# Optimization experiments

Hardware: AMD Instinct MI355X
Metric: run time of the kernel (lower is better)

Reference implementation:

```python
import jax, jax.numpy as jnp
import numpy as np

POOL = 7
SUB = 2
C = 256
NUM_CLASS = 81
N_ROIS = 1000
IMG = 1024


def _roi_align(feat, rois, img_size, pool=POOL, sub=SUB):
    # feat: (1, C, H, W); rois: (N, 4) as (y1, x1, y2, x2) in image coords
    H, W = feat.shape[2], feat.shape[3]
    fhw = jnp.array([H, W, H, W], jnp.float32) - 1.0
    im = jnp.concatenate([img_size, img_size]).astype(jnp.float32) - 1.0
    rif = rois * fhw / im  # rois mapped into feature-map coords
    S = pool * sub  # subsampled grid per axis (14)
    h_step = (rif[:, 2] - rif[:, 0]) / S  # (N,)
    w_step = (rif[:, 3] - rif[:, 1]) / S
    grid = jnp.arange(S, dtype=jnp.float32) + 0.5
    ys = grid[None, :] * h_step[:, None] + rif[:, 0:1]  # (N, S)
    xs = grid[None, :] * w_step[:, None] + rif[:, 1:2]  # (N, S)
    cy = ys[:, :, None]  # (N, S, 1) -> broadcast (N, S, S)
    cx = xs[:, None, :]  # (N, 1, S)
    iu = jnp.floor(cy)
    il = jnp.floor(cx)
    ly = cy - iu  # frac parts (bilinear weights)
    lx = cx - il
    iu = iu.astype(jnp.int32)
    il = il.astype(jnp.int32)
    idn = jnp.ceil(cy).astype(jnp.int32)
    ir = jnp.ceil(cx).astype(jnp.int32)
    iu = jnp.broadcast_to(iu, (rois.shape[0], S, S))
    idn = jnp.broadcast_to(idn, (rois.shape[0], S, S))
    il = jnp.broadcast_to(il, (rois.shape[0], S, S))
    ir = jnp.broadcast_to(ir, (rois.shape[0], S, S))
    f = feat[0]  # (C, H, W)
    # fancy-index gather of 4 corners: each (C, N, S, S)
    pre = (f[:, iu, il] * (1 - ly) * (1 - lx)
           + f[:, idn, il] * ly * (1 - lx)
           + f[:, iu, ir] * (1 - ly) * lx
           + f[:, idn, ir] * ly * lx)
    pre = pre.transpose(1, 0, 2, 3)  # (N, C, S, S)
    N = rois.shape[0]
    post = pre.reshape(N, f.shape[0], pool, sub, pool, sub).max(axis=(3, 5))
    return post  # (N, C, pool, pool)


def _pyramid_roi_pool(feats, rois, img_size):
    h = rois[:, 2] - rois[:, 0] + 1
    w = rois[:, 3] - rois[:, 1] + 1
    lvl = jnp.floor(jnp.log(jnp.sqrt(h * w) / 224.0) / 0.693147 + 4.0)
    lvl = jnp.clip(lvl, 2.0, 5.0)
    # compute ROIAlign against each level, select per-roi by mask
    out = jnp.zeros((rois.shape[0], C, POOL, POOL), jnp.float32)
    for i, l in enumerate(range(2, 6)):
        pooled = _roi_align(feats[i], rois, img_size)
        mask = (lvl == l)[:, None, None, None]
        out = jnp.where(mask, pooled, out)
    return out


def setup_inputs() -> dict:
    key = jax.random.key(0)
    ks = jax.random.split(key, 10)
    feat2 = jax.random.normal(ks[0], (1, C, 256, 256), jnp.float32)
    feat3 = jax.random.normal(ks[1], (1, C, 128, 128), jnp.float32)
    feat4 = jax.random.normal(ks[2], (1, C, 64, 64), jnp.float32)
    feat5 = jax.random.normal(ks[3], (1, C, 32, 32), jnp.float32)
    # valid boxes: log-uniform sizes in [32, 512] to cover levels 2..5
    u = jax.random.uniform(ks[4], (N_ROIS, 4))
    sh = jnp.exp(jnp.log(32.0) + u[:, 0] * (jnp.log(512.0) - jnp.log(32.0)))
    sw = jnp.exp(jnp.log(32.0) + u[:, 1] * (jnp.log(512.0) - jnp.log(32.0)))
    y1 = u[:, 2] * (IMG - 1 - sh)
    x1 = u[:, 3] * (IMG - 1 - sw)
    rois = jnp.stack([y1, x1, y1 + sh, x1 + sw], axis=1).astype(jnp.float32)
    img_size = jnp.array([IMG, IMG], jnp.int32)
    D = C * POOL * POOL  # 12544
    W1 = jax.random.normal(ks[5], (D, 1024), jnp.float32) * 0.01
    b1 = jnp.zeros((1024,), jnp.float32)
    W2 = jax.random.normal(ks[6], (1024, 1024), jnp.float32) * 0.01
    b2 = jnp.zeros((1024,), jnp.float32)
    Wloc = jax.random.normal(ks[7], (1024, NUM_CLASS * 4), jnp.float32) * 0.001
    bloc = jnp.zeros((NUM_CLASS * 4,), jnp.float32)
    Wsc = jax.random.normal(ks[8], (1024, NUM_CLASS), jnp.float32) * 0.01
    bsc = jnp.zeros((NUM_CLASS,), jnp.float32)
    return {"feat2": feat2, "feat3": feat3, "feat4": feat4, "feat5": feat5,
            "rois": rois, "img_size": img_size,
            "W1": W1, "b1": b1, "W2": W2, "b2": b2,
            "Wloc": Wloc, "bloc": bloc, "Wsc": Wsc, "bsc": bsc}


def reference(feat2, feat3, feat4, feat5, rois, img_size,
              W1, b1, W2, b2, Wloc, bloc, Wsc, bsc):
    pooled = _pyramid_roi_pool([feat2, feat3, feat4, feat5], rois, img_size)
    x = pooled.reshape(pooled.shape[0], -1)  # (N, 12544)
    fc = jax.nn.relu(x @ W1 + b1)
    fc = jax.nn.relu(fc @ W2 + b2)
    roi_cls_locs = fc @ Wloc + bloc
    roi_scores = fc @ Wsc + bsc
    return roi_cls_locs, roi_scores
```

## Files before the change

### kernel.cpp

```cpp
#include <hip/hip_runtime.h>
#include <hip/hip_bf16.h>
#include <cstdint>
#include <cstddef>

typedef __bf16 bf16x8 __attribute__((ext_vector_type(8)));
typedef float floatx4 __attribute__((ext_vector_type(4)));

#define NROIS 1000
#define PD    12544
#define K2_1  25088
#define FC_N  1024
#define K2_2  2048
#define NLOC  324
#define NSC   81
#define NH    405

#define OFF_FT   0u
#define OFF_W1T  0u
#define OFF_PART 12845056u
#define OFF_T2   0u
#define OFF_T3   16777216u
#define OFF_T4   20971520u
#define OFF_T5   22020096u
#define OFF_POOL 22282240u
#define OFF_W2T  35127296u
#define OFF_WHT  36175872u
#define OFF_FC1  36700160u
#define OFF_FC2  37748736u

__device__ __forceinline__ unsigned short f2bf(float x) {
    unsigned int u = __float_as_uint(x);
    u = u + 0x7fffu + ((u >> 16) & 1u);
    return (unsigned short)(u >> 16);
}
__device__ __forceinline__ float bf2f(unsigned short h) {
    return __uint_as_float(((unsigned int)h) << 16);
}
__device__ __forceinline__ ushort2 split_hl(float f) {
    const unsigned short hi = f2bf(f);
    const unsigned short lo = f2bf(f - bf2f(hi));
    return make_ushort2(hi, lo);
}

__global__ __launch_bounds__(256) void transpose_feat_kernel(
    const float* __restrict__ f2, const float* __restrict__ f3,
    const float* __restrict__ f4, const float* __restrict__ f5,
    float* __restrict__ fT)
{
    __shared__ float tile[64][65];
    int bx = blockIdx.x;
    const float* src; float* dst; int P;
    if (bx < 1024)      {            src = f2; dst = fT + OFF_T2; P = 65536; }
    else if (bx < 1280) { bx -= 1024; src = f3; dst = fT + OFF_T3; P = 16384; }
    else if (bx < 1344) { bx -= 1280; src = f4; dst = fT + OFF_T4; P = 4096; }
    else                { bx -= 1344; src = f5; dst = fT + OFF_T5; P = 1024; }

    const int p0  = bx * 64;
    const int c0  = blockIdx.y * 64;
    const int col = threadIdx.x & 63;
    const int r0  = threadIdx.x >> 6;
#pragma unroll
    for (int r = r0; r < 64; r += 4)
        tile[r][col] = src[(size_t)(c0 + r) * P + p0 + col];
    __syncthreads();
#pragma unroll
    for (int r = r0; r < 64; r += 4)
        dst[(size_t)(p0 + r) * 256 + c0 + col] = tile[col][r];
}

__global__ __launch_bounds__(256) void roi_pool_kernel(
    const float* __restrict__ fT, const float* __restrict__ rois,
    const int* __restrict__ img_size, ushort2* __restrict__ pooledHL)
{
    const int roi = blockIdx.x;
    const int ph  = blockIdx.y;
    const int c   = threadIdx.x;

    const float y1 = rois[roi * 4 + 0];
    const float x1 = rois[roi * 4 + 1];
    const float y2 = rois[roi * 4 + 2];
    const float x2 = rois[roi * 4 + 3];

    const float hh = y2 - y1 + 1.0f;
    const float ww = x2 - x1 + 1.0f;
    float lvlf = floorf(logf(sqrtf(hh * ww) / 224.0f) / 0.693147f + 4.0f);
    lvlf = fminf(fmaxf(lvlf, 2.0f), 5.0f);
    const int lvl = (int)lvlf;

    const float* f;
    int H;
    if (lvl == 2)      { f = fT + OFF_T2; H = 256; }
    else if (lvl == 3) { f = fT + OFF_T3; H = 128; }
    else if (lvl == 4) { f = fT + OFF_T4; H = 64;  }
    else               { f = fT + OFF_T5; H = 32;  }
    const int W = H;

    const float imh = (float)img_size[0] - 1.0f;
    const float imw = (float)img_size[1] - 1.0f;
    const float r0 = y1 * (float)(H - 1) / imh;
    const float r1 = x1 * (float)(W - 1) / imw;
    const float r2 = y2 * (float)(H - 1) / imh;
    const float r3 = x2 * (float)(W - 1) / imw;
    const float hs  = (r2 - r0) * (1.0f / 14.0f);
    const float wst = (r3 - r1) * (1.0f / 14.0f);

    float m[7];
#pragma unroll
    for (int i = 0; i < 7; ++i) m[i] = -INFINITY;

#pragma unroll
    for (int syy = 0; syy < 2; ++syy) {
        const float cy = ((float)(ph * 2 + syy) + 0.5f) * hs + r0;
        const float fy = floorf(cy);
        int   iu  = (int)fy;
        int   idn = (int)ceilf(cy);
        const float ly = cy - fy;
        iu  = min(max(iu, 0),  H - 1);
        idn = min(max(idn, 0), H - 1);
        const float wU = 1.0f - ly, wD = ly;
        const float* rowU = f + (size_t)(iu  * W) * 256;
        const float* rowD = f + (size_t)(idn * W) * 256;

#pragma unroll
        for (int sx = 0; sx < 14; ++sx) {
            const float cx = ((float)sx + 0.5f) * wst + r1;
            const float fx = floorf(cx);
            int   il = (int)fx;
            int   ir = (int)ceilf(cx);
            const float lx = cx - fx;
            il = min(max(il, 0), W - 1);
            ir = min(max(ir, 0), W - 1);

            const float v00 = rowU[il * 256 + c];
            const float v01 = rowU[ir * 256 + c];
            const float v10 = rowD[il * 256 + c];
            const float v11 = rowD[ir * 256 + c];
            const float v = (v00 * (1.0f - lx) + v01 * lx) * wU
                          + (v10 * (1.0f - lx) + v11 * lx) * wD;
            m[sx >> 1] = fmaxf(m[sx >> 1], v);
        }
    }

    ushort2* outRow = pooledHL + (size_t)roi * PD + c;
#pragma unroll
    for (int pw = 0; pw < 7; ++pw)
        outRow[(ph * 7 + pw) * 256] = split_hl(m[pw]);
}

__global__ __launch_bounds__(256) void convert_w1_kernel(
    const float* __restrict__ W1, ushort2* __restrict__ W1T)
{
    __shared__ float tile[64][65];
    const int p0  = blockIdx.x * 64;
    const int n0  = blockIdx.y * 64;
    const int col = threadIdx.x & 63;
    const int r0  = threadIdx.x >> 6;
#pragma unroll
    for (int r = r0; r < 64; r += 4) {
        const int pp   = p0 + r;
        const int ksrc = (pp & 255) * 49 + (pp >> 8);
        tile[r][col] = W1[(size_t)ksrc * 1024 + n0 + col];
    }
    __syncthreads();
#pragma unroll
    for (int nr = r0; nr < 64; nr += 4)
        W1T[(size_t)(n0 + nr) * PD + p0 + col] = split_hl(tile[col][nr]);
}

__global__ __launch_bounds__(256) void convert_w2h_kernel(
    const float* __restrict__ W2, const float* __restrict__ Wloc,
    const float* __restrict__ Wsc, ushort2* __restrict__ W2T,
    ushort2* __restrict__ WhT)
{
    __shared__ float tile[64][65];
    const int p0  = blockIdx.x * 64;
    const int col = threadIdx.x & 63;
    const int r0  = threadIdx.x >> 6;

    if (blockIdx.y < 16) {
        const int n0 = blockIdx.y * 64;
#pragma unroll
        for (int r = r0; r < 64; r += 4)
            tile[r][col] = W2[(size_t)(p0 + r) * 1024 + n0 + col];
        __syncthreads();
#pragma unroll
        for (int nr = r0; nr < 64; nr += 4)
            W2T[(size_t)(n0 + nr) * 1024 + p0 + col] = split_hl(tile[col][nr]);
    } else {
        const int n0 = (blockIdx.y - 16) * 64;
#pragma unroll
        for (int r = r0; r < 64; r += 4) {
            const int pp = p0 + r;
            const int n  = n0 + col;
            float v = 0.0f;
            if (n < NLOC)    v = Wloc[(size_t)pp * NLOC + n];
            else if (n < NH) v = Wsc[(size_t)pp * NSC + (n - NLOC)];
            tile[r][col] = v;
        }
        __syncthreads();
#pragma unroll
        for (int nr = r0; nr < 64; nr += 4)
            WhT[(size_t)(n0 + nr) * 1024 + p0 + col] = split_hl(tile[col][nr]);
    }
}

__global__ __launch_bounds__(256, 4) void gemm_bf16_kernel(
    const unsigned short* __restrict__ A,
    const unsigned short* __restrict__ B,
    float* __restrict__ partial,
    int K2, int N, int kLen)
{
    __shared__ __align__(16) unsigned short As[64 * 64];
    __shared__ __align__(16) unsigned short Bs[128 * 64];

    const int tid  = threadIdx.x;
    const int lane = tid & 63;
    const int wave = tid >> 6;
    const int kStart = blockIdx.x * kLen;
    const int n0 = blockIdx.y * 128;
    const int m0 = blockIdx.z * 64;

    const int rIn  = lane >> 3;
    const int cSrc = (lane & 7) ^ rIn;

    const int mrow = lane & 15, quad = lane >> 4;

    floatx4 acc[8];
#pragma unroll
    for (int j = 0; j < 8; ++j)
        acc[j] = (floatx4){0.f, 0.f, 0.f, 0.f};

    for (int k0 = kStart; k0 < kStart + kLen; k0 += 64) {
#pragma unroll
        for (int q = 0; q < 2; ++q) {
            const int rowBase = wave * 16 + q * 8;
            const unsigned short* ga =
                A + (size_t)(m0 + rowBase + rIn) * K2 + k0 + cSrc * 8;
            __builtin_amdgcn_global_load_lds(
                (const __attribute__((address_space(1))) void*)ga,
                (__attribute__((address_space(3))) void*)&As[rowBase * 64], 16, 0, 0);
        }
#pragma unroll
        for (int q = 0; q < 4; ++q) {
            const int rowBase = wave * 32 + q * 8;
            const unsigned short* gb =
                B + (size_t)(n0 + rowBase + rIn) * K2 + k0 + cSrc * 8;
            __builtin_amdgcn_global_load_lds(
                (const __attribute__((address_space(1))) void*)gb,
                (__attribute__((address_space(3))) void*)&Bs[rowBase * 64], 16, 0, 0);
        }
        __syncthreads();

#pragma unroll
        for (int ks = 0; ks < 2; ++ks) {
            const int ra = wave * 16 + mrow;
            const int ca = ((ks * 4 + quad) ^ (ra & 7)) * 8;
            const bf16x8 aF = *reinterpret_cast<const bf16x8*>(&As[ra * 64 + ca]);
#pragma unroll
            for (int j = 0; j < 8; ++j) {
                const int rb = j * 16 + mrow;
                const int cb = ((ks * 4 + quad) ^ (rb & 7)) * 8;
                const bf16x8 bF = *reinterpret_cast<const bf16x8*>(&Bs[rb * 64 + cb]);
                acc[j] = __builtin_amdgcn_mfma_f32_16x16x32_bf16(aF, bF, acc[j], 0, 0, 0);
            }
        }
        __syncthreads();
    }

    float* p = partial + (size_t)blockIdx.x * (size_t)(gridDim.z * 64) * N;
    const int row = m0 + wave * 16 + quad * 4;
#pragma unroll
    for (int j = 0; j < 8; ++j) {
        const int col = n0 + j * 16 + mrow;
#pragma unroll
        for (int r = 0; r < 4; ++r)
            p[(size_t)(row + r) * N + col] = acc[j][r];
    }
}

__global__ __launch_bounds__(256) void reduce_fc_kernel(
    const float* __restrict__ partial, const float* __restrict__ bias,
    ushort2* __restrict__ outHL, int nz)
{
    const int i4 = blockIdx.x * 256 + threadIdx.x;
    const int off = i4 * 4;
    const int m = off >> 10, n = off & 1023;
    float4 acc = *reinterpret_cast<const float4*>(partial + off);
    for (int z = 1; z < nz; ++z) {
        const float4 v = *reinterpret_cast<const float4*>(
            partial + (size_t)z * 1024 * 1024 + off);
        acc.x += v.x; acc.y += v.y; acc.z += v.z; acc.w += v.w;
    }
    const float4 bv = *reinterpret_cast<const float4*>(bias + n);
    ushort2* o = outHL + (size_t)m * 1024 + n;
    o[0] = split_hl(fmaxf(acc.x + bv.x, 0.f));
    o[1] = split_hl(fmaxf(acc.y + bv.y, 0.f));
    o[2] = split_hl(fmaxf(acc.z + bv.z, 0.f));
    o[3] = split_hl(fmaxf(acc.w + bv.w, 0.f));
}

__global__ __launch_bounds__(256) void reduce_heads_kernel(
    const float* __restrict__ partial, const float* __restrict__ bloc,
    const float* __restrict__ bsc, float* __restrict__ out0,
    float* __restrict__ out1, int nz)
{
    const int m = blockIdx.x;
    for (int n = threadIdx.x; n < NH; n += 256) {
        float s = 0.f;
        for (int z = 0; z < nz; ++z)
            s += partial[(size_t)z * 1024 * 512 + (size_t)m * 512 + n];
        if (n < NLOC) out0[(size_t)m * NLOC + n] = s + bloc[n];
        else          out1[(size_t)m * NSC + (n - NLOC)] = s + bsc[n - NLOC];
    }
}

extern "C" void kernel_launch(void* const* d_in, const int* in_sizes, int n_in,
                              void* d_out, int out_size, void* d_ws, size_t ws_size,
                              hipStream_t stream)
{
    const float* f2   = (const float*)d_in[0];
    const float* f3   = (const float*)d_in[1];
    const float* f4   = (const float*)d_in[2];
    const float* f5   = (const float*)d_in[3];
    const float* rois = (const float*)d_in[4];
    const int*   img  = (const int*)d_in[5];
    const float* W1   = (const float*)d_in[6];
    const float* b1   = (const float*)d_in[7];
    const float* W2   = (const float*)d_in[8];
    const float* b2   = (const float*)d_in[9];
    const float* Wloc = (const float*)d_in[10];
    const float* bloc = (const float*)d_in[11];
    const float* Wsc  = (const float*)d_in[12];
    const float* bsc  = (const float*)d_in[13];
    float* out = (float*)d_out;

    float* ws = (float*)d_ws;
    float*   fT     = ws + OFF_FT;
    ushort2* pooled = (ushort2*)(ws + OFF_POOL);
    ushort2* w1t    = (ushort2*)(ws + OFF_W1T);
    float*   part   = ws + OFF_PART;
    ushort2* w2t    = (ushort2*)(ws + OFF_W2T);
    ushort2* wht    = (ushort2*)(ws + OFF_WHT);
    ushort2* fc1    = (ushort2*)(ws + OFF_FC1);
    ushort2* fc2    = (ushort2*)(ws + OFF_FC2);

    transpose_feat_kernel<<<dim3(1360, 4), 256, 0, stream>>>(f2, f3, f4, f5, fT);

    roi_pool_kernel<<<dim3(NROIS, 7), 256, 0, stream>>>(fT, rois, img, pooled);

    convert_w1_kernel<<<dim3(196, 16), 256, 0, stream>>>(W1, w1t);
    convert_w2h_kernel<<<dim3(16, 23), 256, 0, stream>>>(W2, Wloc, Wsc, w2t, wht);

    gemm_bf16_kernel<<<dim3(8, 8, 16), 256, 0, stream>>>(
        (const unsigned short*)pooled, (const unsigned short*)w1t, part,
        K2_1, 1024, K2_1 / 8);
    reduce_fc_kernel<<<1024, 256, 0, stream>>>(part, b1, fc1, 8);

    gemm_bf16_kernel<<<dim3(4, 8, 16), 256, 0, stream>>>(
        (const unsigned short*)fc1, (const unsigned short*)w2t, part,
        K2_2, 1024, K2_2 / 4);
    reduce_fc_kernel<<<1024, 256, 0, stream>>>(part, b2, fc2, 4);

    gemm_bf16_kernel<<<dim3(8, 4, 16), 256, 0, stream>>>(
        (const unsigned short*)fc2, (const unsigned short*)wht, part,
        K2_2, 512, K2_2 / 8);
    reduce_heads_kernel<<<NROIS, 256, 0, stream>>>(
        part, bloc, bsc, out, out + (size_t)NROIS * NLOC, 8);
}
```

Baseline: 383.1 us.

## Enlarge GEMM tile to 128x128 and vectorize ROI pooling across waves

The bf16 MFMA GEMM now computes a 128x128 tile per block, with each wave holding a 4x4 grid of 16x16 accumulators, so more data is reused from LDS per fragment load. Launch grids are halved in M, and the FC2 split-K count is raised to 8. The ROI pooling kernel is restructured: each wave handles one y-subsample and one x-parity, loads float4 channel vectors, and max-reduces through shared memory with 16-byte packed stores. The trade-off is higher register and LDS use per block, hence lower occupancy, and an extra barrier in the pooling kernel.

```diff
diff --git a/kernel.cpp b/kernel.cpp
--- a/kernel.cpp
+++ b/kernel.cpp
@@ -72,9 +72,13 @@
     const float* __restrict__ fT, const float* __restrict__ rois,
     const int* __restrict__ img_size, ushort2* __restrict__ pooledHL)
 {
-    const int roi = blockIdx.x;
-    const int ph  = blockIdx.y;
-    const int c   = threadIdx.x;
+    const int roi  = blockIdx.x;
+    const int ph   = blockIdx.y;
+    const int tid  = threadIdx.x;
+    const int lane = tid & 63;
+    const int wave = tid >> 6;
+    const int syy  = wave >> 1;
+    const int sxp  = wave & 1;
 
     const float y1 = rois[roi * 4 + 0];
     const float x1 = rois[roi * 4 + 1];
@@ -104,47 +108,63 @@
     const float hs  = (r2 - r0) * (1.0f / 14.0f);
     const float wst = (r3 - r1) * (1.0f / 14.0f);
 
-    float m[7];
-#pragma unroll
-    for (int i = 0; i < 7; ++i) m[i] = -INFINITY;
-
-#pragma unroll
-    for (int syy = 0; syy < 2; ++syy) {
-        const float cy = ((float)(ph * 2 + syy) + 0.5f) * hs + r0;
-        const float fy = floorf(cy);
-        int   iu  = (int)fy;
-        int   idn = (int)ceilf(cy);
-        const float ly = cy - fy;
-        iu  = min(max(iu, 0),  H - 1);
-        idn = min(max(idn, 0), H - 1);
-        const float wU = 1.0f - ly, wD = ly;
-        const float* rowU = f + (size_t)(iu  * W) * 256;
-        const float* rowD = f + (size_t)(idn * W) * 256;
-
-#pragma unroll
-        for (int sx = 0; sx < 14; ++sx) {
-            const float cx = ((float)sx + 0.5f) * wst + r1;
-            const float fx = floorf(cx);
-            int   il = (int)fx;
-            int   ir = (int)ceilf(cx);
-            const float lx = cx - fx;
-            il = min(max(il, 0), W - 1);
-            ir = min(max(ir, 0), W - 1);
-
-            const float v00 = rowU[il * 256 + c];
-            const float v01 = rowU[ir * 256 + c];
-            const float v10 = rowD[il * 256 + c];
-            const float v11 = rowD[ir * 256 + c];
-            const float v = (v00 * (1.0f - lx) + v01 * lx) * wU
-                          + (v10 * (1.0f - lx) + v11 * lx) * wD;
-            m[sx >> 1] = fmaxf(m[sx >> 1], v);
-        }
-    }
-
-    ushort2* outRow = pooledHL + (size_t)roi * PD + c;
-#pragma unroll
-    for (int pw = 0; pw < 7; ++pw)
-        outRow[(ph * 7 + pw) * 256] = split_hl(m[pw]);
+    const float cy = ((float)(ph * 2 + syy) + 0.5f) * hs + r0;
+    const float fy = floorf(cy);
+    int   iu  = (int)fy;
+    int   idn = (int)ceilf(cy);
+    const float ly = cy - fy;
+    iu  = min(max(iu, 0),  H - 1);
+    idn = min(max(idn, 0), H - 1);
+    const float wU = 1.0f - ly, wD = ly;
+    const float4* rowU = (const float4*)(f + (size_t)(iu  * W) * 256);
+    const float4* rowD = (const float4*)(f + (size_t)(idn * W) * 256);
+
+    __shared__ float4 red[4][7][64];
+
+#pragma unroll
+    for (int pw = 0; pw < 7; ++pw) {
+        const int sx = pw * 2 + sxp;
+        const float cx = ((float)sx + 0.5f) * wst + r1;
+        const float fx = floorf(cx);
+        int   il = (int)fx;
+        int   ir = (int)ceilf(cx);
+        const float lx = cx - fx;
+        il = min(max(il, 0), W - 1);
+        ir = min(max(ir, 0), W - 1);
+
+        const float4 v00 = rowU[il * 64 + lane];
+        const float4 v01 = rowU[ir * 64 + lane];
+        const float4 v10 = rowD[il * 64 + lane];
+        const float4 v11 = rowD[ir * 64 + lane];
+        const float lxm = 1.0f - lx;
+        float4 v;
+        v.x = (v00.x * lxm + v01.x * lx) * wU + (v10.x * lxm + v11.x * lx) * wD;
+        v.y = (v00.y * lxm + v01.y * lx) * wU + (v10.y * lxm + v11.y * lx) * wD;
+        v.z = (v00.z * lxm + v01.z * lx) * wU + (v10.z * lxm + v11.z * lx) * wD;
+        v.w = (v00.w * lxm + v01.w * lx) * wU + (v10.w * lxm + v11.w * lx) * wD;
+        red[wave][pw][lane] = v;
+    }
+    __syncthreads();
+
+    for (int idx = tid; idx < 448; idx += 256) {
+        const int pw = idx >> 6, cg = idx & 63;
+        const float4 a = red[0][pw][cg];
+        const float4 b = red[1][pw][cg];
+        const float4 c = red[2][pw][cg];
+        const float4 d = red[3][pw][cg];
+        float4 mv;
+        mv.x = fmaxf(fmaxf(a.x, b.x), fmaxf(c.x, d.x));
+        mv.y = fmaxf(fmaxf(a.y, b.y), fmaxf(c.y, d.y));
+        mv.z = fmaxf(fmaxf(a.z, b.z), fmaxf(c.z, d.z));
+        mv.w = fmaxf(fmaxf(a.w, b.w), fmaxf(c.w, d.w));
+        union { ushort2 u2[4]; uint4 v4; } pk;
+        pk.u2[0] = split_hl(mv.x);
+        pk.u2[1] = split_hl(mv.y);
+        pk.u2[2] = split_hl(mv.z);
+        pk.u2[3] = split_hl(mv.w);
+        ushort2* outp = pooledHL + (size_t)roi * PD + (ph * 7 + pw) * 256 + cg * 4;
+        *reinterpret_cast<uint4*>(outp) = pk.v4;
+    }
 }
 
 __global__ __launch_bounds__(256) void convert_w1_kernel(
@@ -204,13 +224,13 @@
     }
 }
 
-__global__ __launch_bounds__(256, 4) void gemm_bf16_kernel(
+__global__ __launch_bounds__(256) void gemm_bf16_kernel(
     const unsigned short* __restrict__ A,
     const unsigned short* __restrict__ B,
     float* __restrict__ partial,
     int K2, int N, int kLen)
 {
-    __shared__ __align__(16) unsigned short As[64 * 64];
+    __shared__ __align__(16) unsigned short As[128 * 64];
     __shared__ __align__(16) unsigned short Bs[128 * 64];
 
     const int tid  = threadIdx.x;
@@ -218,22 +238,27 @@
     const int wave = tid >> 6;
     const int kStart = blockIdx.x * kLen;
     const int n0 = blockIdx.y * 128;
-    const int m0 = blockIdx.z * 64;
+    const int m0 = blockIdx.z * 128;
+
+    const int wr = wave >> 1;
+    const int wc = wave & 1;
 
     const int rIn  = lane >> 3;
     const int cSrc = (lane & 7) ^ rIn;
 
     const int mrow = lane & 15, quad = lane >> 4;
 
-    floatx4 acc[8];
-#pragma unroll
-    for (int j = 0; j < 8; ++j)
-        acc[j] = (floatx4){0.f, 0.f, 0.f, 0.f};
+    floatx4 acc[4][4];
+#pragma unroll
+    for (int mi = 0; mi < 4; ++mi)
+#pragma unroll
+        for (int nj = 0; nj < 4; ++nj)
+            acc[mi][nj] = (floatx4){0.f, 0.f, 0.f, 0.f};
 
     for (int k0 = kStart; k0 < kStart + kLen; k0 += 64) {
 #pragma unroll
-        for (int q = 0; q < 2; ++q) {
-            const int rowBase = wave * 16 + q * 8;
+        for (int q = 0; q < 4; ++q) {
+            const int rowBase = wave * 32 + q * 8;
             const unsigned short* ga =
                 A + (size_t)(m0 + rowBase + rIn) * K2 + k0 + cSrc * 8;
             __builtin_amdgcn_global_load_lds(
@@ -253,28 +278,41 @@
 
 #pragma unroll
         for (int ks = 0; ks < 2; ++ks) {
-            const int ra = wave * 16 + mrow;
-            const int ca = ((ks * 4 + quad) ^ (ra & 7)) * 8;
-            const bf16x8 aF = *reinterpret_cast<const bf16x8*>(&As[ra * 64 + ca]);
-#pragma unroll
-            for (int j = 0; j < 8; ++j) {
-                const int rb = j * 16 + mrow;
-                const int cb = ((ks * 4 + quad) ^ (rb & 7)) * 8;
-                const bf16x8 bF = *reinterpret_cast<const bf16x8*>(&Bs[rb * 64 + cb]);
-                acc[j] = __builtin_amdgcn_mfma_f32_16x16x32_bf16(aF, bF, acc[j], 0, 0, 0);
+            const int chunk = ks * 4 + quad;
+            bf16x8 aF[4], bF[4];
+#pragma unroll
+            for (int mi = 0; mi < 4; ++mi) {
+                const int ra = wr * 64 + mi * 16 + mrow;
+                aF[mi] = *reinterpret_cast<const bf16x8*>(
+                    &As[ra * 64 + ((chunk ^ (ra & 7)) * 8)]);
             }
+#pragma unroll
+            for (int nj = 0; nj < 4; ++nj) {
+                const int rb = wc * 64 + nj * 16 + mrow;
+                bF[nj] = *reinterpret_cast<const bf16x8*>(
+                    &Bs[rb * 64 + ((chunk ^ (rb & 7)) * 8)]);
+            }
+#pragma unroll
+            for (int mi = 0; mi < 4; ++mi)
+#pragma unroll
+                for (int nj = 0; nj < 4; ++nj)
+                    acc[mi][nj] = __builtin_amdgcn_mfma_f32_16x16x32_bf16(
+                        aF[mi], bF[nj], acc[mi][nj], 0, 0, 0);
         }
         __syncthreads();
     }
 
-    float* p = partial + (size_t)blockIdx.x * (size_t)(gridDim.z * 64) * N;
-    const int row = m0 + wave * 16 + quad * 4;
-#pragma unroll
-    for (int j = 0; j < 8; ++j) {
-        const int col = n0 + j * 16 + mrow;
-#pragma unroll
-        for (int r = 0; r < 4; ++r)
-            p[(size_t)(row + r) * N + col] = acc[j][r];
+    float* p = partial + (size_t)blockIdx.x * (size_t)(gridDim.z * 128) * N;
+#pragma unroll
+    for (int mi = 0; mi < 4; ++mi) {
+        const int row = m0 + wr * 64 + mi * 16 + quad * 4;
+#pragma unroll
+        for (int nj = 0; nj < 4; ++nj) {
+            const int col = n0 + wc * 64 + nj * 16 + mrow;
+#pragma unroll
+            for (int r = 0; r < 4; ++r)
+                p[(size_t)(row + r) * N + col] = acc[mi][nj][r];
+        }
     }
 }
 
@@ -351,17 +389,17 @@
     convert_w1_kernel<<<dim3(196, 16), 256, 0, stream>>>(W1, w1t);
     convert_w2h_kernel<<<dim3(16, 23), 256, 0, stream>>>(W2, Wloc, Wsc, w2t, wht);
 
-    gemm_bf16_kernel<<<dim3(8, 8, 16), 256, 0, stream>>>(
+    gemm_bf16_kernel<<<dim3(8, 8, 8), 256, 0, stream>>>(
         (const unsigned short*)pooled, (const unsigned short*)w1t, part,
         K2_1, 1024, K2_1 / 8);
     reduce_fc_kernel<<<1024, 256, 0, stream>>>(part, b1, fc1, 8);
 
-    gemm_bf16_kernel<<<dim3(4, 8, 16), 256, 0, stream>>>(
+    gemm_bf16_kernel<<<dim3(8, 8, 8), 256, 0, stream>>>(
         (const unsigned short*)fc1, (const unsigned short*)w2t, part,
-        K2_2, 1024, K2_2 / 4);
-    reduce_fc_kernel<<<1024, 256, 0, stream>>>(part, b2, fc2, 4);
-
-    gemm_bf16_kernel<<<dim3(8, 4, 16), 256, 0, stream>>>(
+        K2_2, 1024, K2_2 / 8);
+    reduce_fc_kernel<<<1024, 256, 0, stream>>>(part, b2, fc2, 8);
+
+    gemm_bf16_kernel<<<dim3(8, 4, 8), 256, 0, stream>>>(
         (const unsigned short*)fc2, (const unsigned short*)wht, part,
         K2_2, 512, K2_2 / 8);
     reduce_heads_kernel<<<NROIS, 256, 0, stream>>>(
```

Measured after the change: 396.9 us. 1.04x slower.
